# Performance work log

Hardware: AMD Instinct MI355X
Metric: run time of the kernel (lower is better)

Reference implementation:

```python
import jax, jax.numpy as jnp
import numpy as np

MEM_SIZE = 2000
FEA_DIM = 256
FMAP = 32
BATCH = 32
SHRINK = 0.0025
EPS = 1e-12


def setup_inputs() -> dict:
    key = jax.random.key(0)
    k1, k2, k3, k4 = jax.random.split(key, 4)
    stdv = 1.0 / np.sqrt(FEA_DIM)
    inp = {
        "input": jax.random.normal(k1, (BATCH, FEA_DIM, FMAP, FMAP), dtype=jnp.float32),
        "label_batch": jax.random.randint(k2, (BATCH,), 0, 2),
        "weight": jax.random.uniform(k3, (MEM_SIZE, FEA_DIM), dtype=jnp.float32, minval=-stdv, maxval=stdv),
        "pos_embedding": jax.random.normal(k4, (1, FEA_DIM, FMAP, FMAP), dtype=jnp.float32),
    }
    return inp


def _forward(x, weight, pos_embedding):
    b, c, h, w = x.shape
    m = weight.shape[0]
    x = x + pos_embedding  # pos=True
    xr = x.transpose(0, 2, 3, 1).reshape(-1, c)  # [b*h*w, c]
    # addressing: linear -> softmax over memory slots
    att = jax.nn.softmax(jnp.einsum('nc,mc->nm', xr, weight), axis=1)  # [N, m]
    # compact loss: MSE to nearest memory item (argmax of att before shrink)
    idx = jnp.argmax(att, axis=1)
    pos_item = weight[idx]  # [N, c]
    compact_loss = jnp.mean((xr - pos_item) ** 2)
    # distance loss: hinge on pairwise squared distances between memory items
    sq = jnp.sum(weight * weight, axis=1)
    d2 = sq[:, None] + sq[None, :] - 2.0 * (weight @ weight.T)  # [m, m]
    dist = 1.0 - d2
    dist = dist * (dist > 0).astype(dist.dtype)
    dist = jnp.triu(dist, k=1)
    distance_loss = dist.sum() * 2.0 / (m * (m - 1))
    # hard shrink relu + L1 normalize (shrink_thres > 0)
    att = jax.nn.relu(att - SHRINK) * att / (jnp.abs(att - SHRINK) + EPS)
    att = att / jnp.maximum(jnp.sum(jnp.abs(att), axis=1, keepdims=True), EPS)
    # memory read
    out = jnp.einsum('nm,mc->nc', att, weight)
    out = out.reshape(b, h, w, c).transpose(0, 3, 1, 2)
    return out, compact_loss, distance_loss


def reference(input, label_batch, weight, pos_embedding):
    return _forward(input, weight, pos_embedding)
```

## Files before the change

kernel.cpp:

```cpp
#include <hip/hip_runtime.h>
#include <hip/hip_bf16.h>

typedef unsigned char u8;
typedef unsigned short u16;
typedef unsigned int u32;
typedef long long s64;
typedef float f32x4 __attribute__((ext_vector_type(4)));
typedef long long s64x2 __attribute__((ext_vector_type(2)));

#define MEM    2000
#define FEA    256
#define SLSTR  2064
#define OSTR   265
#define XRS    264
#define POOLSZ 66048
#define OUTN   8388608
#define LSC2   0.022542108517490387f

__device__ __forceinline__ u32 f2e4m3(float x) {
    float ax = fabsf(x);
    u32 s = (__builtin_bit_cast(u32, x) >> 24) & 0x80u;
    if (ax >= 448.f) return s | 0x7e;
    if (ax < 0.015625f) {
        int q = (int)rintf(ax * 512.f);
        return s | (u32)q;
    }
    int e = (int)(__builtin_bit_cast(u32, ax) >> 23) - 127;
    float scale = __builtin_bit_cast(float, (u32)((127 - e + 3) << 23));
    int q = (int)rintf(ax * scale);
    int E = e + 7;
    if (q == 16) { q = 8; E += 1; if (E > 15) return s | 0x7e; }
    return s | (u32)(E << 3) | (u32)(q & 7);
}

__global__ __launch_bounds__(256) void prep_kernel(const float* __restrict__ W,
                                                   u8* __restrict__ WTc,
                                                   u8* __restrict__ Wc,
                                                   float* __restrict__ sqv,
                                                   float* __restrict__ loss) {
    const int blk = blockIdx.x, t = threadIdx.x;
    const int m0 = blk * 8;
    {
        const int sl = t >> 5, cl = t & 31;
        const int slot = m0 + sl;
        const int ch0 = cl * 8;
        const float* wr = W + slot * 256 + ch0;
        f32x4 v0 = *(const f32x4*)wr;
        f32x4 v1 = *(const f32x4*)(wr + 4);
        float ss = v0[0]*v0[0] + v0[1]*v0[1] + v0[2]*v0[2] + v0[3]*v0[3]
                 + v1[0]*v1[0] + v1[1]*v1[1] + v1[2]*v1[2] + v1[3]*v1[3];
        ss += __shfl_xor(ss, 1); ss += __shfl_xor(ss, 2); ss += __shfl_xor(ss, 4);
        ss += __shfl_xor(ss, 8); ss += __shfl_xor(ss, 16);
        if (cl == 0) sqv[slot] = ss;
        const int c = slot >> 6, s = slot & 63;
        const int kk = cl >> 2, agp = cl & 3;
        const int kp = kk >> 1, klo = kk & 1;
        u32 lo = 0, hi = 0;
#pragma unroll
        for (int i = 0; i < 4; ++i) {
            lo |= f2e4m3(v0[i] * 16.f) << (i * 8);
            hi |= f2e4m3(v1[i] * 16.f) << (i * 8);
        }
        u8* dst = Wc + c * 16384 + (size_t)((kp * 4 + agp) * 64 + s) * 16 + klo * 8;
        *(u32*)dst = lo;
        *(u32*)(dst + 4) = hi;
    }
    {
        const int ch = t;
        const int chunk = m0 >> 6;
        const int kl0 = m0 & 63;
        const int klo = kl0 >> 5, agp = (kl0 & 31) >> 3;
        u32 lo = 0, hi = 0;
#pragma unroll
        for (int i = 0; i < 8; ++i) {
            u32 bb = f2e4m3(W[(m0 + i) * 256 + ch] * 16.f);
            if (i < 4) lo |= bb << (i * 8); else hi |= bb << ((i - 4) * 8);
        }
        u8* dst = WTc + chunk * 16384 + ch * 64 + agp * 16 + klo * 8;
        *(u32*)dst = lo;
        *(u32*)(dst + 4) = hi;
    }
    if (blk == 0 && t == 0) {
        loss[0] = 0.0f;
        loss[1] = -2000.0f / (2000.0f * 1999.0f);
    }
}

__global__ __attribute__((amdgpu_flat_work_group_size(512, 512), amdgpu_waves_per_eu(4, 4)))
void main_kernel(
        const float* __restrict__ inp, const float* __restrict__ posb,
        const u8* __restrict__ Wc, const u8* __restrict__ WTc,
        const float* __restrict__ sqv, float* __restrict__ out,
        float* __restrict__ loss) {
    __shared__ __align__(16) u8 pool[POOLSZ];
    __shared__ float sPM[4][32];
    __shared__ int   sPI[4][32];
    __shared__ float sPZ[4][32];
    __shared__ float sPD[4][32];
    __shared__ float sSS[8][32];
    __shared__ float sMax[32];
    __shared__ float sThr[32];
    __shared__ float sSrw[32];
    __shared__ float sInv[32];

    const int t = threadIdx.x;
    const int w = t >> 6, lane = t & 63;
    const int ar = lane & 15, ag = lane >> 4;
    const int blk = blockIdx.x, b = blk >> 5, hw0 = (blk & 31) << 5;
    const int q = w & 3, rt = w >> 2;
    const int row_a = rt * 16 + ar;

    {
        const int hw = t & 31, cg = t >> 5;
        const float* ip = inp + (size_t)b * 262144 + hw0 + hw;
        const float* pp = posb + hw0 + hw;
        float ss = 0.f;
        u8* xrow = pool + hw * XRS + cg * 16;
#pragma unroll
        for (int j = 0; j < 8; ++j) {
            const int ch = cg * 16 + 2 * j;
            float v0 = ip[ch * 1024] + pp[ch * 1024];
            float v1 = ip[(ch + 1) * 1024] + pp[(ch + 1) * 1024];
            ss += v0 * v0 + v1 * v1;
            u16 pk2 = (u16)(f2e4m3(v0 * 4.f) | (f2e4m3(v1 * 4.f) << 8));
            *(u16*)(xrow + 2 * j) = pk2;
        }
        ss += __shfl_xor(ss, 32);
        if (lane < 32) sSS[w][lane] = ss;
    }
    __syncthreads();

    s64 xB[8];
#pragma unroll
    for (int kk = 0; kk < 8; ++kk)
        xB[kk] = *(const s64*)(pool + row_a * XRS + kk * 32 + ag * 8);

    const u8* wbase = Wc + ag * 1024 + (q * 16 + ar) * 16;

    {
        float bm = -3e38f, z0 = 0.f;
        int bi = 0x7fffffff;
#pragma unroll 4
        for (int c = 0; c < 32; ++c) {
            const u8* p = wbase + c * 16384;
            s64x2 w0 = *(const s64x2*)(p);
            s64x2 w1 = *(const s64x2*)(p + 4096);
            s64x2 w2 = *(const s64x2*)(p + 8192);
            s64x2 w3 = *(const s64x2*)(p + 12288);
            f32x4 a = {0.f, 0.f, 0.f, 0.f};
            a = __builtin_amdgcn_mfma_f32_16x16x32_fp8_fp8(w0[0], xB[0], a, 0, 0, 0);
            a = __builtin_amdgcn_mfma_f32_16x16x32_fp8_fp8(w0[1], xB[1], a, 0, 0, 0);
            a = __builtin_amdgcn_mfma_f32_16x16x32_fp8_fp8(w1[0], xB[2], a, 0, 0, 0);
            a = __builtin_amdgcn_mfma_f32_16x16x32_fp8_fp8(w1[1], xB[3], a, 0, 0, 0);
            a = __builtin_amdgcn_mfma_f32_16x16x32_fp8_fp8(w2[0], xB[4], a, 0, 0, 0);
            a = __builtin_amdgcn_mfma_f32_16x16x32_fp8_fp8(w2[1], xB[5], a, 0, 0, 0);
            a = __builtin_amdgcn_mfma_f32_16x16x32_fp8_fp8(w3[0], xB[6], a, 0, 0, 0);
            a = __builtin_amdgcn_mfma_f32_16x16x32_fp8_fp8(w3[1], xB[7], a, 0, 0, 0);
            if (c == 31 && q != 0) { a[0] = -3e38f; a[1] = -3e38f; a[2] = -3e38f; a[3] = -3e38f; }
            const int cb = (c << 6) + q * 16 + ag * 4;
#pragma unroll
            for (int e = 0; e < 4; ++e) {
                float v = a[e]; int id = cb + e;
                bool g = (v > bm) || (v == bm && id < bi);
                bm = g ? v : bm;
                bi = g ? id : bi;
            }
            z0 += exp2f(a[0] * LSC2) + exp2f(a[1] * LSC2)
                + exp2f(a[2] * LSC2) + exp2f(a[3] * LSC2);
        }
#pragma unroll
        for (int d = 16; d < 64; d <<= 1) {
            float om = __shfl_xor(bm, d);
            int   oi = __shfl_xor(bi, d);
            float oz = __shfl_xor(z0, d);
            bool g = (om > bm) || (om == bm && oi < bi);
            bm = g ? om : bm;
            bi = g ? oi : bi;
            z0 += oz;
        }
        if (lane < 16) {
            sPM[q][rt * 16 + lane] = bm;
            sPI[q][rt * 16 + lane] = bi;
            sPZ[q][rt * 16 + lane] = z0;
        }
    }
    __syncthreads();

    if (t < 32) {
        float M = sPM[0][t]; int I = sPI[0][t];
#pragma unroll
        for (int qq = 1; qq < 4; ++qq) {
            float m2 = sPM[qq][t]; int i2 = sPI[qq][t];
            bool g = (m2 > M) || (m2 == M && i2 < I);
            M = g ? m2 : M; I = g ? i2 : I;
        }
        float z0t = sPZ[0][t] + sPZ[1][t] + sPZ[2][t] + sPZ[3][t];
        sMax[t] = M;
        sThr[t] = 0.0025f * z0t;
        sSrw[t] = 64.f * exp2f(-M * LSC2);
        float ssq = 0.f;
#pragma unroll
        for (int ww = 0; ww < 8; ++ww) ssq += sSS[ww][t];
        float term = ssq - 2.f * (M * (1.0f / 64.0f)) + sqv[I];
#pragma unroll
        for (int d = 1; d < 32; d <<= 1) term += __shfl_xor(term, d);
        if (t == 0) atomicAdd(loss, term * (1.0f / 8388608.0f));
    }
    __syncthreads();

    {
        const float thr0 = sThr[row_a];
        const float Srw  = sSrw[row_a];
        const int newoff = (((q * 2 + (ag >> 1)) & 3) << 4) | ((q >> 1) << 3) | ((ag & 1) << 2);
        const int rowbase = row_a * SLSTR + newoff;
        float denS = 0.f;
#pragma unroll 4
        for (int c = 0; c < 32; ++c) {
            const u8* p = wbase + c * 16384;
            s64x2 w0 = *(const s64x2*)(p);
            s64x2 w1 = *(const s64x2*)(p + 4096);
            s64x2 w2 = *(const s64x2*)(p + 8192);
            s64x2 w3 = *(const s64x2*)(p + 12288);
            f32x4 a = {0.f, 0.f, 0.f, 0.f};
            a = __builtin_amdgcn_mfma_f32_16x16x32_fp8_fp8(w0[0], xB[0], a, 0, 0, 0);
            a = __builtin_amdgcn_mfma_f32_16x16x32_fp8_fp8(w0[1], xB[1], a, 0, 0, 0);
            a = __builtin_amdgcn_mfma_f32_16x16x32_fp8_fp8(w1[0], xB[2], a, 0, 0, 0);
            a = __builtin_amdgcn_mfma_f32_16x16x32_fp8_fp8(w1[1], xB[3], a, 0, 0, 0);
            a = __builtin_amdgcn_mfma_f32_16x16x32_fp8_fp8(w2[0], xB[4], a, 0, 0, 0);
            a = __builtin_amdgcn_mfma_f32_16x16x32_fp8_fp8(w2[1], xB[5], a, 0, 0, 0);
            a = __builtin_amdgcn_mfma_f32_16x16x32_fp8_fp8(w3[0], xB[6], a, 0, 0, 0);
            a = __builtin_amdgcn_mfma_f32_16x16x32_fp8_fp8(w3[1], xB[7], a, 0, 0, 0);
            if (c == 31 && q != 0) { a[0] = -3e38f; a[1] = -3e38f; a[2] = -3e38f; a[3] = -3e38f; }
            float e0 = exp2f(a[0] * LSC2);
            float e1 = exp2f(a[1] * LSC2);
            float e2 = exp2f(a[2] * LSC2);
            float e3 = exp2f(a[3] * LSC2);
            float v0 = e0 > thr0 ? e0 : 0.f;
            float v1 = e1 > thr0 ? e1 : 0.f;
            float v2 = e2 > thr0 ? e2 : 0.f;
            float v3 = e3 > thr0 ? e3 : 0.f;
            denS += v0 + v1 + v2 + v3;
            float f0 = v0 * Srw, f1 = v1 * Srw, f2 = v2 * Srw, f3 = v3 * Srw;
            u32 pk;
            asm("v_cvt_pk_fp8_f32 %0, %1, %2" : "=v"(pk) : "v"(f0), "v"(f1));
            asm("v_cvt_pk_fp8_f32 %0, %1, %2 op_sel:[0,0,1]" : "+v"(pk) : "v"(f2), "v"(f3));
            *(u32*)(pool + rowbase + (c << 6)) = pk;
        }
        denS += __shfl_xor(denS, 16);
        denS += __shfl_xor(denS, 32);
        if (lane < 16) sPD[q][rt * 16 + lane] = denS;
    }
    __syncthreads();
    if (t < 32) {
        float dd = sPD[0][t] + sPD[1][t] + sPD[2][t] + sPD[3][t];
        sInv[t] = dd > 0.f ? exp2f(sMax[t] * LSC2) * (1.0f / 1024.0f) / dd : 0.0f;
    }
    __syncthreads();

    const int ch0 = (w * 2) * 16 + ar;
    const int ch1 = ch0 + 16;
    const u8* sLr0 = pool + ar * SLSTR + ag * 16;
    const u8* sLr1 = pool + (16 + ar) * SLSTR + ag * 16;
    const u8* wt0 = WTc + ch0 * 64 + ag * 16;
    const u8* wt1 = WTc + ch1 * 64 + ag * 16;
    f32x4 o00 = {0.f,0.f,0.f,0.f}, o01 = {0.f,0.f,0.f,0.f};
    f32x4 o10 = {0.f,0.f,0.f,0.f}, o11 = {0.f,0.f,0.f,0.f};
#pragma unroll 4
    for (int c = 0; c < 32; ++c) {
        s64x2 B0 = *(const s64x2*)(wt0 + c * 16384);
        s64x2 B1 = *(const s64x2*)(wt1 + c * 16384);
        s64x2 A0 = *(const s64x2*)(sLr0 + c * 64);
        s64x2 A1 = *(const s64x2*)(sLr1 + c * 64);
        o00 = __builtin_amdgcn_mfma_f32_16x16x32_fp8_fp8(A0[0], B0[0], o00, 0, 0, 0);
        o00 = __builtin_amdgcn_mfma_f32_16x16x32_fp8_fp8(A0[1], B0[1], o00, 0, 0, 0);
        o01 = __builtin_amdgcn_mfma_f32_16x16x32_fp8_fp8(A1[0], B0[0], o01, 0, 0, 0);
        o01 = __builtin_amdgcn_mfma_f32_16x16x32_fp8_fp8(A1[1], B0[1], o01, 0, 0, 0);
        o10 = __builtin_amdgcn_mfma_f32_16x16x32_fp8_fp8(A0[0], B1[0], o10, 0, 0, 0);
        o10 = __builtin_amdgcn_mfma_f32_16x16x32_fp8_fp8(A0[1], B1[1], o10, 0, 0, 0);
        o11 = __builtin_amdgcn_mfma_f32_16x16x32_fp8_fp8(A1[0], B1[0], o11, 0, 0, 0);
        o11 = __builtin_amdgcn_mfma_f32_16x16x32_fp8_fp8(A1[1], B1[1], o11, 0, 0, 0);
    }
    __syncthreads();

    {
        float* sO = (float*)pool;
#pragma unroll
        for (int i = 0; i < 4; ++i) {
            int r0 = ag * 4 + i, r1 = 16 + ag * 4 + i;
            sO[r0 * OSTR + ch0] = o00[i] * sInv[r0];
            sO[r1 * OSTR + ch0] = o01[i] * sInv[r1];
            sO[r0 * OSTR + ch1] = o10[i] * sInv[r0];
            sO[r1 * OSTR + ch1] = o11[i] * sInv[r1];
        }
    }
    __syncthreads();
    {
        const float* sO = (const float*)pool;
        const int hw = t & 31, cq = t >> 5;
        float* op = out + (size_t)b * 262144 + hw0 + hw;
#pragma unroll
        for (int i = 0; i < 16; ++i) {
            int ch = cq + (i << 4);
            op[ch * 1024] = sO[hw * OSTR + ch];
        }
    }
}

__global__ __launch_bounds__(256) void dist_kernel(const u8* __restrict__ Wc,
                                                   const float* __restrict__ sqv,
                                                   float* __restrict__ dl) {
    __shared__ float red[4];
    int t = threadIdx.x, w = t >> 6, lane = t & 63;
    int ar = lane & 15, ag = lane >> 4;
    const int i0 = blockIdx.x << 4;
    const int ci = i0 >> 6, si0 = i0 & 63;
    s64x2 af2[4];
#pragma unroll
    for (int kp = 0; kp < 4; ++kp)
        af2[kp] = *(const s64x2*)(Wc + ci * 16384 + (size_t)((kp * 4 + ag) * 64 + si0 + ar) * 16);
    float sqi[4];
#pragma unroll
    for (int e = 0; e < 4; ++e) sqi[e] = sqv[i0 + ag * 4 + e];
    float sum = 0.f;
    for (int jt = w; jt < 125; jt += 4) {
        const int j0 = jt << 4;
        const int cj = j0 >> 6, sj0 = j0 & 63;
        f32x4 acc = {0.f, 0.f, 0.f, 0.f};
#pragma unroll
        for (int kp = 0; kp < 4; ++kp) {
            s64x2 bf = *(const s64x2*)(Wc + cj * 16384 + (size_t)((kp * 4 + ag) * 64 + sj0 + ar) * 16);
            acc = __builtin_amdgcn_mfma_f32_16x16x32_fp8_fp8(af2[kp][0], bf[0], acc, 0, 0, 0);
            acc = __builtin_amdgcn_mfma_f32_16x16x32_fp8_fp8(af2[kp][1], bf[1], acc, 0, 0, 0);
        }
        float sqj = sqv[j0 + ar];
#pragma unroll
        for (int e = 0; e < 4; ++e) {
            float dist = 1.0f - (sqi[e] + sqj - acc[e] * 0.0078125f);
            sum += dist > 0.f ? dist : 0.f;
        }
    }
#pragma unroll
    for (int d = 1; d < 64; d <<= 1) sum += __shfl_xor(sum, d);
    if (lane == 0) red[w] = sum;
    __syncthreads();
    if (t == 0) {
        float s = red[0] + red[1] + red[2] + red[3];
        atomicAdd(dl, s * (1.0f / (2000.0f * 1999.0f)));
    }
}

extern "C" void kernel_launch(void* const* d_in, const int* in_sizes, int n_in,
                              void* d_out, int out_size, void* d_ws, size_t ws_size,
                              hipStream_t stream) {
    (void)in_sizes; (void)n_in; (void)out_size; (void)ws_size;
    const float* inp  = (const float*)d_in[0];
    const float* W    = (const float*)d_in[2];
    const float* posb = (const float*)d_in[3];
    float* out = (float*)d_out;

    u8* WTc = (u8*)d_ws;
    u8* Wc  = (u8*)d_ws + 524288;
    float* sqv = (float*)((u8*)d_ws + 1048576);

    hipLaunchKernelGGL(prep_kernel, dim3(250), dim3(256), 0, stream, W, WTc, Wc, sqv, out + OUTN);
    hipLaunchKernelGGL(main_kernel, dim3(1024), dim3(512), 0, stream, inp, posb, Wc, WTc, sqv, out, out + OUTN);
    hipLaunchKernelGGL(dist_kernel, dim3(125), dim3(256), 0, stream, Wc, sqv, out + OUTN + 1);
}
```

Before: 152.6 us.

## Halve rows per block, split memory chunks across waves, raise occupancy

Each block now handles 16 spatial positions instead of 32, giving twice as many blocks. The 8 waves now split the 32 memory chunks among themselves rather than splitting rows, and the reductions are changed to match. LDS use drops, so the waves-per-EU hint goes from 4 to 6 for higher occupancy. The input fp8 conversion also moves to the hardware v_cvt_pk_fp8_f32 instruction. The trade-off is that each fp8 weight fragment fetched from global memory now feeds only 16 rows, so total weight traffic per output doubles.

```diff
diff --git a/kernel.cpp b/kernel.cpp
--- a/kernel.cpp
+++ b/kernel.cpp
@@ -10,10 +10,12 @@
 
 #define MEM    2000
 #define FEA    256
+#define ROWS   16
 #define SLSTR  2064
 #define OSTR   265
 #define XRS    264
-#define POOLSZ 66048
+#define XBASE  33024
+#define POOLSZ 37248
 #define OUTN   8388608
 #define LSC2   0.022542108517490387f
 
@@ -86,87 +88,94 @@
     }
 }
 
-__global__ __attribute__((amdgpu_flat_work_group_size(512, 512), amdgpu_waves_per_eu(4, 4)))
+__global__ __attribute__((amdgpu_flat_work_group_size(512, 512), amdgpu_waves_per_eu(6, 6)))
 void main_kernel(
         const float* __restrict__ inp, const float* __restrict__ posb,
         const u8* __restrict__ Wc, const u8* __restrict__ WTc,
         const float* __restrict__ sqv, float* __restrict__ out,
         float* __restrict__ loss) {
     __shared__ __align__(16) u8 pool[POOLSZ];
-    __shared__ float sPM[4][32];
-    __shared__ int   sPI[4][32];
-    __shared__ float sPZ[4][32];
-    __shared__ float sPD[4][32];
-    __shared__ float sSS[8][32];
-    __shared__ float sMax[32];
-    __shared__ float sThr[32];
-    __shared__ float sSrw[32];
-    __shared__ float sInv[32];
+    __shared__ float sPM[8][16];
+    __shared__ int   sPI[8][16];
+    __shared__ float sPZ[8][16];
+    __shared__ float sPD[8][16];
+    __shared__ float sSS[8][16];
+    __shared__ float sMax[16];
+    __shared__ float sThr[16];
+    __shared__ float sSrw[16];
+    __shared__ float sInv[16];
 
     const int t = threadIdx.x;
     const int w = t >> 6, lane = t & 63;
     const int ar = lane & 15, ag = lane >> 4;
-    const int blk = blockIdx.x, b = blk >> 5, hw0 = (blk & 31) << 5;
-    const int q = w & 3, rt = w >> 2;
-    const int row_a = rt * 16 + ar;
-
-    {
-        const int hw = t & 31, cg = t >> 5;
+    const int blk = blockIdx.x, b = blk >> 6, hw0 = (blk & 63) << 4;
+
+    {
+        const int hw = t & 15, cg = t >> 4;
         const float* ip = inp + (size_t)b * 262144 + hw0 + hw;
         const float* pp = posb + hw0 + hw;
         float ss = 0.f;
-        u8* xrow = pool + hw * XRS + cg * 16;
-#pragma unroll
-        for (int j = 0; j < 8; ++j) {
-            const int ch = cg * 16 + 2 * j;
-            float v0 = ip[ch * 1024] + pp[ch * 1024];
-            float v1 = ip[(ch + 1) * 1024] + pp[(ch + 1) * 1024];
+        u8* xrow = pool + XBASE + hw * XRS + cg * 8;
+#pragma unroll
+        for (int j = 0; j < 4; ++j) {
+            const int ch = cg * 8 + 2 * j;
+            float v0 = (ip[ch * 1024] + pp[ch * 1024]) * 4.f;
+            float v1 = (ip[(ch + 1) * 1024] + pp[(ch + 1) * 1024]) * 4.f;
             ss += v0 * v0 + v1 * v1;
-            u16 pk2 = (u16)(f2e4m3(v0 * 4.f) | (f2e4m3(v1 * 4.f) << 8));
-            *(u16*)(xrow + 2 * j) = pk2;
-        }
+            u32 pk;
+            asm("v_cvt_pk_fp8_f32 %0, %1, %2" : "=v"(pk) : "v"(v0), "v"(v1));
+            *(u16*)(xrow + 2 * j) = (u16)pk;
+        }
+        ss *= 0.0625f;
+        ss += __shfl_xor(ss, 16);
         ss += __shfl_xor(ss, 32);
-        if (lane < 32) sSS[w][lane] = ss;
+        if (lane < 16) sSS[w][lane] = ss;
     }
     __syncthreads();
 
     s64 xB[8];
 #pragma unroll
     for (int kk = 0; kk < 8; ++kk)
-        xB[kk] = *(const s64*)(pool + row_a * XRS + kk * 32 + ag * 8);
-
-    const u8* wbase = Wc + ag * 1024 + (q * 16 + ar) * 16;
+        xB[kk] = *(const s64*)(pool + XBASE + ar * XRS + kk * 32 + ag * 8);
+
+    const u8* wfrag = Wc + ag * 1024 + ar * 16;
 
     {
         float bm = -3e38f, z0 = 0.f;
         int bi = 0x7fffffff;
-#pragma unroll 4
-        for (int c = 0; c < 32; ++c) {
-            const u8* p = wbase + c * 16384;
-            s64x2 w0 = *(const s64x2*)(p);
-            s64x2 w1 = *(const s64x2*)(p + 4096);
-            s64x2 w2 = *(const s64x2*)(p + 8192);
-            s64x2 w3 = *(const s64x2*)(p + 12288);
-            f32x4 a = {0.f, 0.f, 0.f, 0.f};
-            a = __builtin_amdgcn_mfma_f32_16x16x32_fp8_fp8(w0[0], xB[0], a, 0, 0, 0);
-            a = __builtin_amdgcn_mfma_f32_16x16x32_fp8_fp8(w0[1], xB[1], a, 0, 0, 0);
-            a = __builtin_amdgcn_mfma_f32_16x16x32_fp8_fp8(w1[0], xB[2], a, 0, 0, 0);
-            a = __builtin_amdgcn_mfma_f32_16x16x32_fp8_fp8(w1[1], xB[3], a, 0, 0, 0);
-            a = __builtin_amdgcn_mfma_f32_16x16x32_fp8_fp8(w2[0], xB[4], a, 0, 0, 0);
-            a = __builtin_amdgcn_mfma_f32_16x16x32_fp8_fp8(w2[1], xB[5], a, 0, 0, 0);
-            a = __builtin_amdgcn_mfma_f32_16x16x32_fp8_fp8(w3[0], xB[6], a, 0, 0, 0);
-            a = __builtin_amdgcn_mfma_f32_16x16x32_fp8_fp8(w3[1], xB[7], a, 0, 0, 0);
-            if (c == 31 && q != 0) { a[0] = -3e38f; a[1] = -3e38f; a[2] = -3e38f; a[3] = -3e38f; }
-            const int cb = (c << 6) + q * 16 + ag * 4;
-#pragma unroll
-            for (int e = 0; e < 4; ++e) {
-                float v = a[e]; int id = cb + e;
-                bool g = (v > bm) || (v == bm && id < bi);
-                bm = g ? v : bm;
-                bi = g ? id : bi;
+#pragma unroll
+        for (int ci = 0; ci < 4; ++ci) {
+            const int c = w + ci * 8;
+            const u8* pcb = wfrag + (size_t)c * 16384;
+            const bool last = (c == 31);
+#pragma unroll
+            for (int sg = 0; sg < 4; ++sg) {
+                const u8* p = pcb + sg * 256;
+                s64x2 w0 = *(const s64x2*)(p);
+                s64x2 w1 = *(const s64x2*)(p + 4096);
+                s64x2 w2 = *(const s64x2*)(p + 8192);
+                s64x2 w3 = *(const s64x2*)(p + 12288);
+                f32x4 a = {0.f, 0.f, 0.f, 0.f};
+                a = __builtin_amdgcn_mfma_f32_16x16x32_fp8_fp8(w0[0], xB[0], a, 0, 0, 0);
+                a = __builtin_amdgcn_mfma_f32_16x16x32_fp8_fp8(w0[1], xB[1], a, 0, 0, 0);
+                a = __builtin_amdgcn_mfma_f32_16x16x32_fp8_fp8(w1[0], xB[2], a, 0, 0, 0);
+                a = __builtin_amdgcn_mfma_f32_16x16x32_fp8_fp8(w1[1], xB[3], a, 0, 0, 0);
+                a = __builtin_amdgcn_mfma_f32_16x16x32_fp8_fp8(w2[0], xB[4], a, 0, 0, 0);
+                a = __builtin_amdgcn_mfma_f32_16x16x32_fp8_fp8(w2[1], xB[5], a, 0, 0, 0);
+                a = __builtin_amdgcn_mfma_f32_16x16x32_fp8_fp8(w3[0], xB[6], a, 0, 0, 0);
+                a = __builtin_amdgcn_mfma_f32_16x16x32_fp8_fp8(w3[1], xB[7], a, 0, 0, 0);
+                if (last && sg != 0) { a[0] = -3e38f; a[1] = -3e38f; a[2] = -3e38f; a[3] = -3e38f; }
+                const int cb = (c << 6) + sg * 16 + ag * 4;
+#pragma unroll
+                for (int e = 0; e < 4; ++e) {
+                    float v = a[e]; int id = cb + e;
+                    bool g = (v > bm) || (v == bm && id < bi);
+                    bm = g ? v : bm;
+                    bi = g ? id : bi;
+                }
+                z0 += exp2f(a[0] * LSC2) + exp2f(a[1] * LSC2)
+                    + exp2f(a[2] * LSC2) + exp2f(a[3] * LSC2);
             }
-            z0 += exp2f(a[0] * LSC2) + exp2f(a[1] * LSC2)
-                + exp2f(a[2] * LSC2) + exp2f(a[3] * LSC2);
         }
 #pragma unroll
         for (int d = 16; d < 64; d <<= 1) {
@@ -179,22 +188,23 @@
             z0 += oz;
         }
         if (lane < 16) {
-            sPM[q][rt * 16 + lane] = bm;
-            sPI[q][rt * 16 + lane] = bi;
-            sPZ[q][rt * 16 + lane] = z0;
-        }
-    }
-    __syncthreads();
-
-    if (t < 32) {
+            sPM[w][lane] = bm;
+            sPI[w][lane] = bi;
+            sPZ[w][lane] = z0;
+        }
+    }
+    __syncthreads();
+
+    if (t < 16) {
         float M = sPM[0][t]; int I = sPI[0][t];
-#pragma unroll
-        for (int qq = 1; qq < 4; ++qq) {
-            float m2 = sPM[qq][t]; int i2 = sPI[qq][t];
+        float z0t = sPZ[0][t];
+#pragma unroll
+        for (int ww = 1; ww < 8; ++ww) {
+            float m2 = sPM[ww][t]; int i2 = sPI[ww][t];
             bool g = (m2 > M) || (m2 == M && i2 < I);
             M = g ? m2 : M; I = g ? i2 : I;
-        }
-        float z0t = sPZ[0][t] + sPZ[1][t] + sPZ[2][t] + sPZ[3][t];
+            z0t += sPZ[ww][t];
+        }
         sMax[t] = M;
         sThr[t] = 0.0025f * z0t;
         sSrw[t] = 64.f * exp2f(-M * LSC2);
@@ -203,104 +213,103 @@
         for (int ww = 0; ww < 8; ++ww) ssq += sSS[ww][t];
         float term = ssq - 2.f * (M * (1.0f / 64.0f)) + sqv[I];
 #pragma unroll
-        for (int d = 1; d < 32; d <<= 1) term += __shfl_xor(term, d);
+        for (int d = 1; d < 16; d <<= 1) term += __shfl_xor(term, d);
         if (t == 0) atomicAdd(loss, term * (1.0f / 8388608.0f));
     }
     __syncthreads();
 
     {
-        const float thr0 = sThr[row_a];
-        const float Srw  = sSrw[row_a];
-        const int newoff = (((q * 2 + (ag >> 1)) & 3) << 4) | ((q >> 1) << 3) | ((ag & 1) << 2);
-        const int rowbase = row_a * SLSTR + newoff;
+        const float thr0 = sThr[ar];
+        const float Srw  = sSrw[ar];
+        const int rowb = ar * SLSTR;
         float denS = 0.f;
-#pragma unroll 4
-        for (int c = 0; c < 32; ++c) {
-            const u8* p = wbase + c * 16384;
-            s64x2 w0 = *(const s64x2*)(p);
-            s64x2 w1 = *(const s64x2*)(p + 4096);
-            s64x2 w2 = *(const s64x2*)(p + 8192);
-            s64x2 w3 = *(const s64x2*)(p + 12288);
-            f32x4 a = {0.f, 0.f, 0.f, 0.f};
-            a = __builtin_amdgcn_mfma_f32_16x16x32_fp8_fp8(w0[0], xB[0], a, 0, 0, 0);
-            a = __builtin_amdgcn_mfma_f32_16x16x32_fp8_fp8(w0[1], xB[1], a, 0, 0, 0);
-            a = __builtin_amdgcn_mfma_f32_16x16x32_fp8_fp8(w1[0], xB[2], a, 0, 0, 0);
-            a = __builtin_amdgcn_mfma_f32_16x16x32_fp8_fp8(w1[1], xB[3], a, 0, 0, 0);
-            a = __builtin_amdgcn_mfma_f32_16x16x32_fp8_fp8(w2[0], xB[4], a, 0, 0, 0);
-            a = __builtin_amdgcn_mfma_f32_16x16x32_fp8_fp8(w2[1], xB[5], a, 0, 0, 0);
-            a = __builtin_amdgcn_mfma_f32_16x16x32_fp8_fp8(w3[0], xB[6], a, 0, 0, 0);
-            a = __builtin_amdgcn_mfma_f32_16x16x32_fp8_fp8(w3[1], xB[7], a, 0, 0, 0);
-            if (c == 31 && q != 0) { a[0] = -3e38f; a[1] = -3e38f; a[2] = -3e38f; a[3] = -3e38f; }
-            float e0 = exp2f(a[0] * LSC2);
-            float e1 = exp2f(a[1] * LSC2);
-            float e2 = exp2f(a[2] * LSC2);
-            float e3 = exp2f(a[3] * LSC2);
-            float v0 = e0 > thr0 ? e0 : 0.f;
-            float v1 = e1 > thr0 ? e1 : 0.f;
-            float v2 = e2 > thr0 ? e2 : 0.f;
-            float v3 = e3 > thr0 ? e3 : 0.f;
-            denS += v0 + v1 + v2 + v3;
-            float f0 = v0 * Srw, f1 = v1 * Srw, f2 = v2 * Srw, f3 = v3 * Srw;
-            u32 pk;
-            asm("v_cvt_pk_fp8_f32 %0, %1, %2" : "=v"(pk) : "v"(f0), "v"(f1));
-            asm("v_cvt_pk_fp8_f32 %0, %1, %2 op_sel:[0,0,1]" : "+v"(pk) : "v"(f2), "v"(f3));
-            *(u32*)(pool + rowbase + (c << 6)) = pk;
+#pragma unroll
+        for (int ci = 0; ci < 4; ++ci) {
+            const int c = w + ci * 8;
+            const u8* pcb = wfrag + (size_t)c * 16384;
+            const bool last = (c == 31);
+#pragma unroll
+            for (int sg = 0; sg < 4; ++sg) {
+                const u8* p = pcb + sg * 256;
+                s64x2 w0 = *(const s64x2*)(p);
+                s64x2 w1 = *(const s64x2*)(p + 4096);
+                s64x2 w2 = *(const s64x2*)(p + 8192);
+                s64x2 w3 = *(const s64x2*)(p + 12288);
+                f32x4 a = {0.f, 0.f, 0.f, 0.f};
+                a = __builtin_amdgcn_mfma_f32_16x16x32_fp8_fp8(w0[0], xB[0], a, 0, 0, 0);
+                a = __builtin_amdgcn_mfma_f32_16x16x32_fp8_fp8(w0[1], xB[1], a, 0, 0, 0);
+                a = __builtin_amdgcn_mfma_f32_16x16x32_fp8_fp8(w1[0], xB[2], a, 0, 0, 0);
+                a = __builtin_amdgcn_mfma_f32_16x16x32_fp8_fp8(w1[1], xB[3], a, 0, 0, 0);
+                a = __builtin_amdgcn_mfma_f32_16x16x32_fp8_fp8(w2[0], xB[4], a, 0, 0, 0);
+                a = __builtin_amdgcn_mfma_f32_16x16x32_fp8_fp8(w2[1], xB[5], a, 0, 0, 0);
+                a = __builtin_amdgcn_mfma_f32_16x16x32_fp8_fp8(w3[0], xB[6], a, 0, 0, 0);
+                a = __builtin_amdgcn_mfma_f32_16x16x32_fp8_fp8(w3[1], xB[7], a, 0, 0, 0);
+                if (last && sg != 0) { a[0] = -3e38f; a[1] = -3e38f; a[2] = -3e38f; a[3] = -3e38f; }
+                float e0 = exp2f(a[0] * LSC2);
+                float e1 = exp2f(a[1] * LSC2);
+                float e2 = exp2f(a[2] * LSC2);
+                float e3 = exp2f(a[3] * LSC2);
+                float v0 = e0 > thr0 ? e0 : 0.f;
+                float v1 = e1 > thr0 ? e1 : 0.f;
+                float v2 = e2 > thr0 ? e2 : 0.f;
+                float v3 = e3 > thr0 ? e3 : 0.f;
+                denS += v0 + v1 + v2 + v3;
+                float f0 = v0 * Srw, f1 = v1 * Srw, f2 = v2 * Srw, f3 = v3 * Srw;
+                u32 pk;
+                asm("v_cvt_pk_fp8_f32 %0, %1, %2" : "=v"(pk) : "v"(f0), "v"(f1));
+                asm("v_cvt_pk_fp8_f32 %0, %1, %2 op_sel:[0,0,1]" : "+v"(pk) : "v"(f2), "v"(f3));
+                const int newoff = (((sg * 2 + (ag >> 1)) & 3) << 4) | ((sg >> 1) << 3) | ((ag & 1) << 2);
+                *(u32*)(pool + rowb + (c << 6) + newoff) = pk;
+            }
         }
         denS += __shfl_xor(denS, 16);
         denS += __shfl_xor(denS, 32);
-        if (lane < 16) sPD[q][rt * 16 + lane] = denS;
-    }
-    __syncthreads();
-    if (t < 32) {
-        float dd = sPD[0][t] + sPD[1][t] + sPD[2][t] + sPD[3][t];
+        if (lane < 16) sPD[w][lane] = denS;
+    }
+    __syncthreads();
+    if (t < 16) {
+        float dd = 0.f;
+#pragma unroll
+        for (int ww = 0; ww < 8; ++ww) dd += sPD[ww][t];
         sInv[t] = dd > 0.f ? exp2f(sMax[t] * LSC2) * (1.0f / 1024.0f) / dd : 0.0f;
     }
     __syncthreads();
 
-    const int ch0 = (w * 2) * 16 + ar;
+    const int ch0 = w * 32 + ar;
     const int ch1 = ch0 + 16;
-    const u8* sLr0 = pool + ar * SLSTR + ag * 16;
-    const u8* sLr1 = pool + (16 + ar) * SLSTR + ag * 16;
+    const u8* sLr = pool + ar * SLSTR + ag * 16;
     const u8* wt0 = WTc + ch0 * 64 + ag * 16;
     const u8* wt1 = WTc + ch1 * 64 + ag * 16;
-    f32x4 o00 = {0.f,0.f,0.f,0.f}, o01 = {0.f,0.f,0.f,0.f};
-    f32x4 o10 = {0.f,0.f,0.f,0.f}, o11 = {0.f,0.f,0.f,0.f};
+    f32x4 o0 = {0.f, 0.f, 0.f, 0.f}, o1 = {0.f, 0.f, 0.f, 0.f};
 #pragma unroll 4
     for (int c = 0; c < 32; ++c) {
+        s64x2 A  = *(const s64x2*)(sLr + c * 64);
         s64x2 B0 = *(const s64x2*)(wt0 + c * 16384);
         s64x2 B1 = *(const s64x2*)(wt1 + c * 16384);
-        s64x2 A0 = *(const s64x2*)(sLr0 + c * 64);
-        s64x2 A1 = *(const s64x2*)(sLr1 + c * 64);
-        o00 = __builtin_amdgcn_mfma_f32_16x16x32_fp8_fp8(A0[0], B0[0], o00, 0, 0, 0);
-        o00 = __builtin_amdgcn_mfma_f32_16x16x32_fp8_fp8(A0[1], B0[1], o00, 0, 0, 0);
-        o01 = __builtin_amdgcn_mfma_f32_16x16x32_fp8_fp8(A1[0], B0[0], o01, 0, 0, 0);
-        o01 = __builtin_amdgcn_mfma_f32_16x16x32_fp8_fp8(A1[1], B0[1], o01, 0, 0, 0);
-        o10 = __builtin_amdgcn_mfma_f32_16x16x32_fp8_fp8(A0[0], B1[0], o10, 0, 0, 0);
-        o10 = __builtin_amdgcn_mfma_f32_16x16x32_fp8_fp8(A0[1], B1[1], o10, 0, 0, 0);
-        o11 = __builtin_amdgcn_mfma_f32_16x16x32_fp8_fp8(A1[0], B1[0], o11, 0, 0, 0);
-        o11 = __builtin_amdgcn_mfma_f32_16x16x32_fp8_fp8(A1[1], B1[1], o11, 0, 0, 0);
+        o0 = __builtin_amdgcn_mfma_f32_16x16x32_fp8_fp8(A[0], B0[0], o0, 0, 0, 0);
+        o0 = __builtin_amdgcn_mfma_f32_16x16x32_fp8_fp8(A[1], B0[1], o0, 0, 0, 0);
+        o1 = __builtin_amdgcn_mfma_f32_16x16x32_fp8_fp8(A[0], B1[0], o1, 0, 0, 0);
+        o1 = __builtin_amdgcn_mfma_f32_16x16x32_fp8_fp8(A[1], B1[1], o1, 0, 0, 0);
     }
     __syncthreads();
 
     {
         float* sO = (float*)pool;
 #pragma unroll
-        for (int i = 0; i < 4; ++i) {
-            int r0 = ag * 4 + i, r1 = 16 + ag * 4 + i;
-            sO[r0 * OSTR + ch0] = o00[i] * sInv[r0];
-            sO[r1 * OSTR + ch0] = o01[i] * sInv[r1];
-            sO[r0 * OSTR + ch1] = o10[i] * sInv[r0];
-            sO[r1 * OSTR + ch1] = o11[i] * sInv[r1];
+        for (int e = 0; e < 4; ++e) {
+            const int r = ag * 4 + e;
+            sO[r * OSTR + ch0] = o0[e] * sInv[r];
+            sO[r * OSTR + ch1] = o1[e] * sInv[r];
         }
     }
     __syncthreads();
     {
         const float* sO = (const float*)pool;
-        const int hw = t & 31, cq = t >> 5;
+        const int hw = t & 15, cq = t >> 4;
         float* op = out + (size_t)b * 262144 + hw0 + hw;
 #pragma unroll
-        for (int i = 0; i < 16; ++i) {
-            int ch = cq + (i << 4);
+        for (int i = 0; i < 8; ++i) {
+            const int ch = cq + 32 * i;
             op[ch * 1024] = sO[hw * OSTR + ch];
         }
     }
@@ -363,6 +372,6 @@
     float* sqv = (float*)((u8*)d_ws + 1048576);
 
     hipLaunchKernelGGL(prep_kernel, dim3(250), dim3(256), 0, stream, W, WTc, Wc, sqv, out + OUTN);
-    hipLaunchKernelGGL(main_kernel, dim3(1024), dim3(512), 0, stream, inp, posb, Wc, WTc, sqv, out, out + OUTN);
+    hipLaunchKernelGGL(main_kernel, dim3(2048), dim3(512), 0, stream, inp, posb, Wc, WTc, sqv, out, out + OUTN);
     hipLaunchKernelGGL(dist_kernel, dim3(125), dim3(256), 0, stream, Wc, sqv, out + OUTN + 1);
 }
```

Measured after the change: 387.2 us. 2.54x slower.
